# Performance work log

Hardware: AMD Instinct MI355X
Metric: run time of the kernel (lower is better)

## Reference

```python
import jax, jax.numpy as jnp
import numpy as np

N_NODES = 100000
D = 128
N_EDGES = 640000


def _spmm(edge_index, w, x, n):
    # out[i] = sum over edges (i<-j): w * x[j]
    src, dst = edge_index[0], edge_index[1]
    return jax.ops.segment_sum(w[:, None] * x[dst], src, num_segments=n)


def setup_inputs() -> dict:
    key = jax.random.key(0)
    ks = jax.random.split(key, 8)
    inp = {
        "index_vectors": jax.random.normal(ks[0], (N_NODES, D), dtype=jnp.float32),
        "edge_index1": jax.random.randint(ks[1], (2, N_EDGES), 0, N_NODES, dtype=jnp.int64),
        "w1": jnp.ones((N_EDGES,), dtype=jnp.float32),
        "edge_index2": jax.random.randint(ks[2], (2, N_EDGES), 0, N_NODES, dtype=jnp.int64),
        "w2": jnp.ones((N_EDGES,), dtype=jnp.float32),
        "edge_index3": jax.random.randint(ks[3], (2, N_EDGES), 0, N_NODES, dtype=jnp.int64),
        "w3": jnp.ones((N_EDGES,), dtype=jnp.float32),
        "zeroth": jax.random.uniform(ks[4], (1, 1), dtype=jnp.float32),
        "fst": jax.random.uniform(ks[5], (1, 1), dtype=jnp.float32),
        "snd": jax.random.uniform(ks[6], (1, 1), dtype=jnp.float32),
        "trd": jax.random.uniform(ks[7], (1, 1), dtype=jnp.float32),
    }
    return inp


def reference(index_vectors, edge_index1, w1, edge_index2, w2, edge_index3, w3,
              zeroth, fst, snd, trd):
    n = index_vectors.shape[0]
    # hop-1 context: A @ x
    fst_ctx = _spmm(edge_index1, w1, index_vectors, n)
    # hop-2 context: A^2 @ roll(x, 1, axis=1)   (permute_vecs=True)
    snd_ctx = _spmm(edge_index2, w2, jnp.roll(index_vectors, 1, axis=1), n)
    # hop-3 context: A^3 @ roll(x, 2, axis=1)
    trd_ctx = _spmm(edge_index3, w3, jnp.roll(index_vectors, 2, axis=1), n)

    # relu-normalized scalar order weights (get_orders)
    r0, r1, r2, r3 = (jax.nn.relu(zeroth), jax.nn.relu(fst),
                      jax.nn.relu(snd), jax.nn.relu(trd))
    tot = r0 + r1 + r2 + r3 + 1e-6
    r0, r1, r2, r3 = r0 / tot, r1 / tot, r2 / tot, r3 / tot

    # use_sign=False -> plain weighted combination
    return r0 * index_vectors + r1 * fst_ctx + r2 * snd_ctx + r3 * trd_ctx
```

## Files before the change

### kernel.cpp

```cpp
#include <hip/hip_runtime.h>

#define N_NODES 100000
#define D 128
#define N_EDGES 640000
#define TOT_EDGES (3 * N_EDGES)

#define NB   256
#define NPB  391
#define BCAP 9216
#define OVF_CAP 16384
#define EPB  3072
#define BINA_BLOCKS (TOT_EDGES / EPB)
#define EPT  (EPB / 256)
#define NKEY 2048

#define WS_OVFCNT 0
#define WS_BCUR   64
#define WS_BBASE  16448
#define WS_BNUM   17472
#define WS_OVF    18496
#define WS_TMP    280640
#define WS_FREC   19155008
#define WS_OFFS   34515008
#define WS_XB     34915016
#define WS_TOTAL_FAST 60515016

#ifndef __has_builtin
#define __has_builtin(x) 0
#endif
#if __has_builtin(__builtin_amdgcn_alignbit)
#define ALIGN16(hi, lo) __builtin_amdgcn_alignbit((hi), (lo), 16)
#else
#define ALIGN16(hi, lo) (((hi) << 16) | ((lo) >> 16))
#endif

__device__ __forceinline__ void load_r(const float* z0, const float* z1,
                                       const float* z2, const float* z3,
                                       float& r0, float& r1, float& r2, float& r3) {
    r0 = fmaxf(z0[0], 0.0f);
    r1 = fmaxf(z1[0], 0.0f);
    r2 = fmaxf(z2[0], 0.0f);
    r3 = fmaxf(z3[0], 0.0f);
    float inv = 1.0f / (r0 + r1 + r2 + r3 + 1e-6f);
    r0 *= inv; r1 *= inv; r2 *= inv; r3 *= inv;
}

__device__ __forceinline__ unsigned short bf16rn(float f) {
    unsigned int u = __float_as_uint(f);
    u += 0x7FFFu + ((u >> 16) & 1u);
    return (unsigned short)(u >> 16);
}

__global__ void cast_kernel(const float* __restrict__ x, ushort* __restrict__ xb) {
    int i = blockIdx.x * 256 + threadIdx.x;
    if (i >= N_NODES * D / 4) return;
    float4 v = ((const float4*)x)[i];
    ushort4 h;
    h.x = bf16rn(v.x); h.y = bf16rn(v.y); h.z = bf16rn(v.z); h.w = bf16rn(v.w);
    ((ushort4*)xb)[i] = h;
}

__global__ void binA_kernel(const int* __restrict__ ei1, const float* __restrict__ w1,
                            const int* __restrict__ ei2, const float* __restrict__ w2,
                            const int* __restrict__ ei3, const float* __restrict__ w3,
                            const float* __restrict__ z0, const float* __restrict__ z1,
                            const float* __restrict__ z2, const float* __restrict__ z3,
                            int* __restrict__ bcur, int* __restrict__ ovf_count,
                            int4* __restrict__ ovf, int2* __restrict__ tmp) {
    __shared__ int hist[NB];
    __shared__ int base[NB];
    int t = threadIdx.x;
    hist[t] = 0;
    __syncthreads();

    float r0, r1, r2, r3;
    load_r(z0, z1, z2, z3, r0, r1, r2, r3);

    int e0 = blockIdx.x * EPB;
    int rank[EPT];
    int bkt[EPT];
    int rxv[EPT];
    float scv[EPT];

#pragma unroll
    for (int k = 0; k < EPT; ++k) {
        int e = e0 + t + k * 256;
        int set = e / N_EDGES;
        int idx = e - set * N_EDGES;
        const int* ei;  const float* w;  float rk;
        if      (set == 0) { ei = ei1; w = w1; rk = r1; }
        else if (set == 1) { ei = ei2; w = w2; rk = r2; }
        else               { ei = ei3; w = w3; rk = r3; }
        int src = ei[idx];
        int dst = ei[N_EDGES + idx];
        int b = src / NPB;
        int local = src - b * NPB;
        bkt[k]  = b;
        rxv[k]  = dst | (set << 17) | (local << 19);
        scv[k]  = rk * w[idx];
        rank[k] = atomicAdd(&hist[b], 1);
    }
    __syncthreads();

    {
        int h = hist[t];
        base[t] = h ? atomicAdd(&bcur[t * 16], h) : 0;
    }
    __syncthreads();

#pragma unroll
    for (int k = 0; k < EPT; ++k) {
        int b = bkt[k];
        int pos = base[b] + rank[k];
        if (pos < BCAP) {
            tmp[(size_t)b * BCAP + pos] = make_int2(rxv[k], __float_as_int(scv[k]));
        } else {
            int o = atomicAdd(ovf_count, 1);
            int src = b * NPB + ((rxv[k] >> 19) & 0x1FF);
            if (o < OVF_CAP) ovf[o] = make_int4(src, rxv[k] & 0x7FFFF,
                                                __float_as_int(scv[k]), 0);
        }
    }
}

__global__ void scanB_kernel(const int* __restrict__ bcur,
                             int* __restrict__ bbase, int* __restrict__ bnum,
                             int* __restrict__ offsets) {
    __shared__ int s[NB];
    int t = threadIdx.x;
    int n = bcur[t * 16];
    if (n > BCAP) n = BCAP;
    bnum[t] = n;
    s[t] = n;
    __syncthreads();
    for (int off = 1; off < NB; off <<= 1) {
        int v = (t >= off) ? s[t - off] : 0;
        __syncthreads();
        s[t] += v;
        __syncthreads();
    }
    bbase[t] = s[t] - n;
    if (t == NB - 1) offsets[N_NODES] = s[t];
}

__global__ void binB_kernel(const int2* __restrict__ tmp,
                            const int* __restrict__ bbase, const int* __restrict__ bnum,
                            int2* __restrict__ frecs, int* __restrict__ offsets) {
    __shared__ int d[NKEY];
    __shared__ int ts[256];
    __shared__ int cur[NKEY];
    int b = blockIdx.x;
    int t = threadIdx.x;
    int n = bnum[b];
    int gbase = bbase[b];

    for (int i = t; i < NKEY; i += 256) d[i] = 0;
    __syncthreads();
    for (int i = t; i < n; i += 256) {
        int rx = tmp[(size_t)b * BCAP + i].x;
        int key = (((rx >> 19) & 0x1FF) << 2) | ((rx >> 17) & 3);
        atomicAdd(&d[key], 1);
    }
    __syncthreads();

    int loc[8];
    int tot = 0;
#pragma unroll
    for (int k = 0; k < 8; ++k) { loc[k] = tot; tot += d[8 * t + k]; }
    ts[t] = tot;
    __syncthreads();
    for (int off = 1; off < 256; off <<= 1) {
        int v = (t >= off) ? ts[t - off] : 0;
        __syncthreads();
        ts[t] += v;
        __syncthreads();
    }
    int tbase = ts[t] - tot;
#pragma unroll
    for (int k = 0; k < 8; ++k) cur[8 * t + k] = tbase + loc[k];
    __syncthreads();

    int node0 = b * NPB;
    for (int l = t; l < NPB; l += 256) {
        int node = node0 + l;
        if (node < N_NODES) offsets[node] = gbase + cur[l << 2];
    }
    __syncthreads();

    for (int i = t; i < n; i += 256) {
        int2 rec = tmp[(size_t)b * BCAP + i];
        int key = (((rec.x >> 19) & 0x1FF) << 2) | ((rec.x >> 17) & 3);
        int pos = atomicAdd(&cur[key], 1);
        frecs[gbase + pos] = make_int2(rec.x & 0x7FFFF, rec.y);
    }
}

#define GB_ACCUM(RX, RY)                                                       \
    {                                                                          \
        const uint4* rowp = (const uint4*)(xb + (size_t)((RX) & 0x1FFFF) * D); \
        uint4 v = rowp[l16];                                                   \
        int sh = ((RX) >> 17) & 3;                                             \
        float sc = __int_as_float(RY);                                         \
        unsigned int pw = (unsigned int)__shfl((int)v.w, prevq);               \
        unsigned int s1x = ALIGN16(v.x, pw);                                   \
        unsigned int s1y = ALIGN16(v.y, v.x);                                  \
        unsigned int s1z = ALIGN16(v.z, v.y);                                  \
        unsigned int s1w = ALIGN16(v.w, v.z);                                  \
        unsigned int u0 = (sh == 0) ? v.x : (sh == 1) ? s1x : pw;              \
        unsigned int u1 = (sh == 0) ? v.y : (sh == 1) ? s1y : v.x;             \
        unsigned int u2 = (sh == 0) ? v.z : (sh == 1) ? s1z : v.y;             \
        unsigned int u3 = (sh == 0) ? v.w : (sh == 1) ? s1w : v.z;             \
        acc0 += sc * __uint_as_float(u0 << 16);                                \
        acc1 += sc * __uint_as_float(u0 & 0xFFFF0000u);                        \
        acc2 += sc * __uint_as_float(u1 << 16);                                \
        acc3 += sc * __uint_as_float(u1 & 0xFFFF0000u);                        \
        acc4 += sc * __uint_as_float(u2 << 16);                                \
        acc5 += sc * __uint_as_float(u2 & 0xFFFF0000u);                        \
        acc6 += sc * __uint_as_float(u3 << 16);                                \
        acc7 += sc * __uint_as_float(u3 & 0xFFFF0000u);                        \
    }

__global__ void gatherb_kernel(const float* __restrict__ x,
                               const ushort* __restrict__ xb,
                               const int* __restrict__ offsets,
                               const int2* __restrict__ recs,
                               const float* __restrict__ z0, const float* __restrict__ z1,
                               const float* __restrict__ z2, const float* __restrict__ z3,
                               float* __restrict__ out) {
    int wid  = (blockIdx.x * blockDim.x + threadIdx.x) >> 6;
    int lane = threadIdx.x & 63;
    if (wid >= N_NODES) return;

    float r0, r1, r2, r3;
    load_r(z0, z1, z2, z3, r0, r1, r2, r3);

    int qt    = lane >> 4;
    int l16   = lane & 15;
    int prevq = (qt << 4) | ((l16 + 15) & 15);

    int beg = offsets[wid];
    int end = offsets[wid + 1];
    int count = end - beg;
    int cnt64 = (count < 64) ? count : 64;

    int mrx = 0, mry = 0;
    if (lane < cnt64) { int2 rec = recs[beg + lane]; mrx = rec.x; mry = rec.y; }

    float acc0 = 0.f, acc1 = 0.f, acc2 = 0.f, acc3 = 0.f;
    float acc4 = 0.f, acc5 = 0.f, acc6 = 0.f, acc7 = 0.f;

    for (int j = 0; j < cnt64; j += 4) {
        int srcl = j + qt;
        int rx = __shfl(mrx, srcl);
        int ry = __shfl(mry, srcl);
        GB_ACCUM(rx, ry)
    }
    for (int q = 64; q < count; q += 4) {
        int qq = q + qt;
        int rx = 0, ry = 0;
        if (qq < count) { int2 rec = recs[beg + qq]; rx = rec.x; ry = rec.y; }
        GB_ACCUM(rx, ry)
    }

    acc0 += __shfl_xor(acc0, 16); acc0 += __shfl_xor(acc0, 32);
    acc1 += __shfl_xor(acc1, 16); acc1 += __shfl_xor(acc1, 32);
    acc2 += __shfl_xor(acc2, 16); acc2 += __shfl_xor(acc2, 32);
    acc3 += __shfl_xor(acc3, 16); acc3 += __shfl_xor(acc3, 32);
    acc4 += __shfl_xor(acc4, 16); acc4 += __shfl_xor(acc4, 32);
    acc5 += __shfl_xor(acc5, 16); acc5 += __shfl_xor(acc5, 32);
    acc6 += __shfl_xor(acc6, 16); acc6 += __shfl_xor(acc6, 32);
    acc7 += __shfl_xor(acc7, 16); acc7 += __shfl_xor(acc7, 32);

    if (lane < 16) {
        const float4* xr = (const float4*)(x + (size_t)wid * D);
        float4 xlo = xr[2 * l16];
        float4 xhi = xr[2 * l16 + 1];
        float4 olo, ohi;
        olo.x = r0 * xlo.x + acc0;
        olo.y = r0 * xlo.y + acc1;
        olo.z = r0 * xlo.z + acc2;
        olo.w = r0 * xlo.w + acc3;
        ohi.x = r0 * xhi.x + acc4;
        ohi.y = r0 * xhi.y + acc5;
        ohi.z = r0 * xhi.z + acc6;
        ohi.w = r0 * xhi.w + acc7;
        float4* op = (float4*)(out + (size_t)wid * D);
        op[2 * l16]     = olo;
        op[2 * l16 + 1] = ohi;
    }
}

__global__ void ovf_kernel(const float* __restrict__ x,
                           const int* __restrict__ ovf_count,
                           const int4* __restrict__ ovf,
                           float* __restrict__ out) {
    int total_waves = (gridDim.x * blockDim.x) >> 6;
    int gw   = (blockIdx.x * blockDim.x + threadIdx.x) >> 6;
    int lane = threadIdx.x & 63;
    int n = *ovf_count;
    if (n > OVF_CAP) n = OVF_CAP;
    for (int r = gw; r < n; r += total_waves) {
        int4 rec = ovf[r];
        int src = rec.x;
        int dst = rec.y & 0x1FFFF;
        int sh  = (rec.y >> 17) & 3;
        float sc = __int_as_float(rec.z);
        const float* xr = x + (size_t)dst * D;
        float* orow = out + (size_t)src * D;
        int c0 = 2 * lane, c1 = 2 * lane + 1;
        atomicAdd(&orow[c0], sc * xr[(c0 - sh) & 127]);
        atomicAdd(&orow[c1], sc * xr[(c1 - sh) & 127]);
    }
}

#define SCAN_BLOCKS ((N_NODES + 255) / 256)
#define WS_COUNTS   0
#define WS_OFFSETS  400000
#define WS_CURSORS  800008
#define WS_BSUM     1200008
#define WS_BPRE     1201576
#define WS_RECS     1203144
#define WS_NEEDED_MID (WS_RECS + (size_t)TOT_EDGES * 8)

__global__ void hist_kernel(const int* __restrict__ ei1, const int* __restrict__ ei2,
                            const int* __restrict__ ei3, int* __restrict__ counts) {
    int e = blockIdx.x * blockDim.x + threadIdx.x;
    if (e >= TOT_EDGES) return;
    int set = e / N_EDGES;
    int idx = e - set * N_EDGES;
    const int* ei = (set == 0) ? ei1 : (set == 1) ? ei2 : ei3;
    atomicAdd(&counts[ei[idx]], 1);
}

__global__ void scan1_kernel(const int* __restrict__ counts,
                             int* __restrict__ offsets, int* __restrict__ bsum) {
    __shared__ int s[256];
    int t = threadIdx.x;
    int i = blockIdx.x * 256 + t;
    int v = (i < N_NODES) ? counts[i] : 0;
    s[t] = v;
    __syncthreads();
    for (int off = 1; off < 256; off <<= 1) {
        int u = (t >= off) ? s[t - off] : 0;
        __syncthreads();
        s[t] += u;
        __syncthreads();
    }
    if (i < N_NODES) offsets[i] = s[t] - v;
    if (t == 255) bsum[blockIdx.x] = s[255];
}

__global__ void scan2_kernel(const int* __restrict__ bsum, int* __restrict__ bpre) {
    __shared__ int s[512];
    int t = threadIdx.x;
    int v = (t < SCAN_BLOCKS) ? bsum[t] : 0;
    s[t] = v;
    __syncthreads();
    for (int off = 1; off < 512; off <<= 1) {
        int u = (t >= off) ? s[t - off] : 0;
        __syncthreads();
        s[t] += u;
        __syncthreads();
    }
    if (t < SCAN_BLOCKS) bpre[t] = s[t] - v;
}

__global__ void scan3_kernel(int* __restrict__ offsets, const int* __restrict__ bpre,
                             int* __restrict__ cursors) {
    int i = blockIdx.x * 256 + threadIdx.x;
    if (i < N_NODES) {
        int v = offsets[i] + bpre[blockIdx.x];
        offsets[i] = v;
        cursors[i] = v;
    }
    if (i == 0) offsets[N_NODES] = TOT_EDGES;
}

__global__ void fill_kernel(const int* __restrict__ ei1, const float* __restrict__ w1,
                            const int* __restrict__ ei2, const float* __restrict__ w2,
                            const int* __restrict__ ei3, const float* __restrict__ w3,
                            const float* __restrict__ z0, const float* __restrict__ z1,
                            const float* __restrict__ z2, const float* __restrict__ z3,
                            int* __restrict__ cursors, int2* __restrict__ recs) {
    int e = blockIdx.x * blockDim.x + threadIdx.x;
    if (e >= TOT_EDGES) return;
    int set = e / N_EDGES;
    int idx = e - set * N_EDGES;
    const int* ei;  const float* w;
    if      (set == 0) { ei = ei1; w = w1; }
    else if (set == 1) { ei = ei2; w = w2; }
    else               { ei = ei3; w = w3; }
    float r0, r1, r2, r3;
    load_r(z0, z1, z2, z3, r0, r1, r2, r3);
    float rk = (set == 0) ? r1 : (set == 1) ? r2 : r3;
    int src = ei[idx];
    int dst = ei[N_EDGES + idx];
    float scale = rk * w[idx];
    int pos = atomicAdd(&cursors[src], 1);
    recs[pos] = make_int2(dst | (set << 17), __float_as_int(scale));
}

__global__ void gatherd_kernel(const float* __restrict__ x,
                               const int* __restrict__ offsets,
                               const int2* __restrict__ recs,
                               const float* __restrict__ z0, const float* __restrict__ z1,
                               const float* __restrict__ z2, const float* __restrict__ z3,
                               float* __restrict__ out) {
    int wid  = (blockIdx.x * blockDim.x + threadIdx.x) >> 6;
    int lane = threadIdx.x & 63;
    if (wid >= N_NODES) return;
    float r0, r1, r2, r3;
    load_r(z0, z1, z2, z3, r0, r1, r2, r3);
    float2 xv = ((const float2*)(x + (size_t)wid * D))[lane];
    int beg = offsets[wid];
    int end = offsets[wid + 1];
    float2 a0 = {0.f, 0.f}, a1 = {0.f, 0.f}, a2 = {0.f, 0.f};
    for (int j = beg; j < end; ++j) {
        int2 rec = recs[j];
        float2 v = ((const float2*)(x + (size_t)(rec.x & 0x1FFFF) * D))[lane];
        int sh = (rec.x >> 17) & 3;
        float sc = __int_as_float(rec.y);
        if      (sh == 0) { a0.x += sc * v.x; a0.y += sc * v.y; }
        else if (sh == 1) { a1.x += sc * v.x; a1.y += sc * v.y; }
        else               { a2.x += sc * v.x; a2.y += sc * v.y; }
    }
    int prev = (lane + 63) & 63;
    float r1y = __shfl(a1.y, prev);
    float r2x = __shfl(a2.x, prev);
    float r2y = __shfl(a2.y, prev);
    float2 o;
    o.x = r0 * xv.x + a0.x + r1y  + r2x;
    o.y = r0 * xv.y + a0.y + a1.x + r2y;
    ((float2*)(out + (size_t)wid * D))[lane] = o;
}

extern "C" void kernel_launch(void* const* d_in, const int* in_sizes, int n_in,
                              void* d_out, int out_size, void* d_ws, size_t ws_size,
                              hipStream_t stream) {
    const float* x   = (const float*)d_in[0];
    const int*   ei1 = (const int*)  d_in[1];
    const float* w1  = (const float*)d_in[2];
    const int*   ei2 = (const int*)  d_in[3];
    const float* w2  = (const float*)d_in[4];
    const int*   ei3 = (const int*)  d_in[5];
    const float* w3  = (const float*)d_in[6];
    const float* z0  = (const float*)d_in[7];
    const float* z1  = (const float*)d_in[8];
    const float* z2  = (const float*)d_in[9];
    const float* z3  = (const float*)d_in[10];
    float* out = (float*)d_out;
    char* wsc = (char*)d_ws;

    if (ws_size >= WS_TOTAL_FAST) {
        int*    ovf_count = (int*)   (wsc + WS_OVFCNT);
        int*    bcur      = (int*)   (wsc + WS_BCUR);
        int*    bbase     = (int*)   (wsc + WS_BBASE);
        int*    bnum      = (int*)   (wsc + WS_BNUM);
        int4*   ovf       = (int4*)  (wsc + WS_OVF);
        int2*   tmp       = (int2*)  (wsc + WS_TMP);
        int2*   frecs     = (int2*)  (wsc + WS_FREC);
        int*    offsets   = (int*)   (wsc + WS_OFFS);
        ushort* xb        = (ushort*)(wsc + WS_XB);

        hipMemsetAsync(wsc, 0, WS_BBASE, stream);
        cast_kernel<<<(N_NODES * D / 4 + 255) / 256, 256, 0, stream>>>(x, xb);
        binA_kernel<<<BINA_BLOCKS, 256, 0, stream>>>(ei1, w1, ei2, w2, ei3, w3,
                                                     z0, z1, z2, z3,
                                                     bcur, ovf_count, ovf, tmp);
        scanB_kernel<<<1, NB, 0, stream>>>(bcur, bbase, bnum, offsets);
        binB_kernel<<<NB, 256, 0, stream>>>(tmp, bbase, bnum, frecs, offsets);
        gatherb_kernel<<<(N_NODES * 64 + 255) / 256, 256, 0, stream>>>(x, xb, offsets,
                                                                       frecs, z0, z1, z2, z3,
                                                                       out);
        ovf_kernel<<<128, 256, 0, stream>>>(x, ovf_count, ovf, out);
    } else {
        int*  counts  = (int*) (wsc + WS_COUNTS);
        int*  offsets = (int*) (wsc + WS_OFFSETS);
        int*  cursors = (int*) (wsc + WS_CURSORS);
        int*  bsum    = (int*) (wsc + WS_BSUM);
        int*  bpre    = (int*) (wsc + WS_BPRE);
        int2* recs    = (int2*)(wsc + WS_RECS);

        hipMemsetAsync(counts, 0, N_NODES * sizeof(int), stream);
        hist_kernel<<<TOT_EDGES / 256, 256, 0, stream>>>(ei1, ei2, ei3, counts);
        scan1_kernel<<<SCAN_BLOCKS, 256, 0, stream>>>(counts, offsets, bsum);
        scan2_kernel<<<1, 512, 0, stream>>>(bsum, bpre);
        scan3_kernel<<<SCAN_BLOCKS, 256, 0, stream>>>(offsets, bpre, cursors);
        fill_kernel<<<TOT_EDGES / 256, 256, 0, stream>>>(ei1, w1, ei2, w2, ei3, w3,
                                                         z0, z1, z2, z3, cursors, recs);
        gatherd_kernel<<<(N_NODES * 64 + 255) / 256, 256, 0, stream>>>(x, offsets, recs,
                                                                       z0, z1, z2, z3, out);
    }
}
```

Before: 280.3 us.

## Fuse cast into binning, fold scan into binB, use finer buckets, unroll gather

The bf16 cast and the first binning pass now run as one launch. The single-block bucket scan is removed and each binB block recomputes the prefix over bucket counts itself. Buckets grow from 256 to 1024, each holding fewer nodes, which spreads the sort across more, smaller blocks. The gather loop now issues two row loads per iteration to raise memory-level parallelism. Together these cut two launches and serial passes, at the cost of redundant scans in every binB block and more global atomics during binning.

```diff
diff --git a/kernel.cpp b/kernel.cpp
--- a/kernel.cpp
+++ b/kernel.cpp
@@ -5,25 +5,24 @@
 #define N_EDGES 640000
 #define TOT_EDGES (3 * N_EDGES)
 
-#define NB   256
-#define NPB  391
-#define BCAP 9216
+#define NB   1024
+#define NPB  98
+#define BCAP 2304
 #define OVF_CAP 16384
 #define EPB  3072
 #define BINA_BLOCKS (TOT_EDGES / EPB)
 #define EPT  (EPB / 256)
-#define NKEY 2048
+#define NKEY 512
+#define CAST_BLOCKS ((N_NODES * D / 4 + 255) / 256)
 
 #define WS_OVFCNT 0
 #define WS_BCUR   64
-#define WS_BBASE  16448
-#define WS_BNUM   17472
-#define WS_OVF    18496
-#define WS_TMP    280640
-#define WS_FREC   19155008
-#define WS_OFFS   34515008
-#define WS_XB     34915016
-#define WS_TOTAL_FAST 60515016
+#define WS_OVF    65600
+#define WS_TMP    327744
+#define WS_FREC   19202112
+#define WS_OFFS   34562112
+#define WS_XB     34962120
+#define WS_TOTAL_FAST 60562120
 
 #ifndef __has_builtin
 #define __has_builtin(x) 0
@@ -51,26 +50,29 @@
     return (unsigned short)(u >> 16);
 }
 
-__global__ void cast_kernel(const float* __restrict__ x, ushort* __restrict__ xb) {
-    int i = blockIdx.x * 256 + threadIdx.x;
-    if (i >= N_NODES * D / 4) return;
-    float4 v = ((const float4*)x)[i];
-    ushort4 h;
-    h.x = bf16rn(v.x); h.y = bf16rn(v.y); h.z = bf16rn(v.z); h.w = bf16rn(v.w);
-    ((ushort4*)xb)[i] = h;
-}
-
-__global__ void binA_kernel(const int* __restrict__ ei1, const float* __restrict__ w1,
-                            const int* __restrict__ ei2, const float* __restrict__ w2,
-                            const int* __restrict__ ei3, const float* __restrict__ w3,
-                            const float* __restrict__ z0, const float* __restrict__ z1,
-                            const float* __restrict__ z2, const float* __restrict__ z3,
-                            int* __restrict__ bcur, int* __restrict__ ovf_count,
-                            int4* __restrict__ ovf, int2* __restrict__ tmp) {
+__global__ __launch_bounds__(256) void prep_kernel(
+        const float* __restrict__ x, ushort* __restrict__ xb,
+        const int* __restrict__ ei1, const float* __restrict__ w1,
+        const int* __restrict__ ei2, const float* __restrict__ w2,
+        const int* __restrict__ ei3, const float* __restrict__ w3,
+        const float* __restrict__ z0, const float* __restrict__ z1,
+        const float* __restrict__ z2, const float* __restrict__ z3,
+        int* __restrict__ bcur, int* __restrict__ ovf_count,
+        int4* __restrict__ ovf, int2* __restrict__ tmp) {
+    if (blockIdx.x >= BINA_BLOCKS) {
+        int i = (blockIdx.x - BINA_BLOCKS) * 256 + threadIdx.x;
+        if (i < N_NODES * D / 4) {
+            float4 v = ((const float4*)x)[i];
+            ushort4 h;
+            h.x = bf16rn(v.x); h.y = bf16rn(v.y); h.z = bf16rn(v.z); h.w = bf16rn(v.w);
+            ((ushort4*)xb)[i] = h;
+        }
+        return;
+    }
     __shared__ int hist[NB];
     __shared__ int base[NB];
     int t = threadIdx.x;
-    hist[t] = 0;
+    for (int i = t; i < NB; i += 256) hist[i] = 0;
     __syncthreads();
 
     float r0, r1, r2, r3;
@@ -102,9 +104,9 @@
     }
     __syncthreads();
 
-    {
-        int h = hist[t];
-        base[t] = h ? atomicAdd(&bcur[t * 16], h) : 0;
+    for (int i = t; i < NB; i += 256) {
+        int h = hist[i];
+        base[i] = h ? atomicAdd(&bcur[i * 16], h) : 0;
     }
     __syncthreads();
 
@@ -116,57 +118,64 @@
             tmp[(size_t)b * BCAP + pos] = make_int2(rxv[k], __float_as_int(scv[k]));
         } else {
             int o = atomicAdd(ovf_count, 1);
-            int src = b * NPB + ((rxv[k] >> 19) & 0x1FF);
+            int src = b * NPB + ((rxv[k] >> 19) & 0x7F);
             if (o < OVF_CAP) ovf[o] = make_int4(src, rxv[k] & 0x7FFFF,
                                                 __float_as_int(scv[k]), 0);
         }
     }
 }
 
-__global__ void scanB_kernel(const int* __restrict__ bcur,
-                             int* __restrict__ bbase, int* __restrict__ bnum,
-                             int* __restrict__ offsets) {
-    __shared__ int s[NB];
-    int t = threadIdx.x;
-    int n = bcur[t * 16];
-    if (n > BCAP) n = BCAP;
-    bnum[t] = n;
-    s[t] = n;
-    __syncthreads();
-    for (int off = 1; off < NB; off <<= 1) {
-        int v = (t >= off) ? s[t - off] : 0;
-        __syncthreads();
-        s[t] += v;
-        __syncthreads();
-    }
-    bbase[t] = s[t] - n;
-    if (t == NB - 1) offsets[N_NODES] = s[t];
-}
-
-__global__ void binB_kernel(const int2* __restrict__ tmp,
-                            const int* __restrict__ bbase, const int* __restrict__ bnum,
-                            int2* __restrict__ frecs, int* __restrict__ offsets) {
+__global__ __launch_bounds__(256) void binB_kernel(
+        const int* __restrict__ bcur, const int2* __restrict__ tmp,
+        int2* __restrict__ frecs, int* __restrict__ offsets) {
+    __shared__ int sc4[256];
     __shared__ int d[NKEY];
     __shared__ int ts[256];
     __shared__ int cur[NKEY];
+    __shared__ int sh_gbase, sh_n;
     int b = blockIdx.x;
     int t = threadIdx.x;
-    int n = bnum[b];
-    int gbase = bbase[b];
-
-    for (int i = t; i < NKEY; i += 256) d[i] = 0;
-    __syncthreads();
+
+    d[t] = 0; d[t + 256] = 0;
+
+    int v4[4];
+    int cex[4];
+    int tsum = 0;
+#pragma unroll
+    for (int k = 0; k < 4; ++k) {
+        int g = 4 * t + k;
+        int v = bcur[g * 16];
+        if (v > BCAP) v = BCAP;
+        cex[k] = tsum;
+        tsum += v;
+        v4[k] = v;
+    }
+    sc4[t] = tsum;
+    __syncthreads();
+    for (int off = 1; off < 256; off <<= 1) {
+        int v = (t >= off) ? sc4[t - off] : 0;
+        __syncthreads();
+        sc4[t] += v;
+        __syncthreads();
+    }
+    if (t == (b >> 2)) {
+        sh_gbase = sc4[t] - tsum + cex[b & 3];
+        sh_n     = v4[b & 3];
+    }
+    if (b == NB - 1 && t == 255) offsets[N_NODES] = sc4[255];
+    __syncthreads();
+    int gbase = sh_gbase;
+    int n     = sh_n;
+
     for (int i = t; i < n; i += 256) {
         int rx = tmp[(size_t)b * BCAP + i].x;
-        int key = (((rx >> 19) & 0x1FF) << 2) | ((rx >> 17) & 3);
+        int key = (((rx >> 19) & 0x7F) << 2) | ((rx >> 17) & 3);
         atomicAdd(&d[key], 1);
     }
     __syncthreads();
 
-    int loc[8];
-    int tot = 0;
-#pragma unroll
-    for (int k = 0; k < 8; ++k) { loc[k] = tot; tot += d[8 * t + k]; }
+    int k0 = d[2 * t], k1 = d[2 * t + 1];
+    int tot = k0 + k1;
     ts[t] = tot;
     __syncthreads();
     for (int off = 1; off < 256; off <<= 1) {
@@ -176,40 +185,37 @@
         __syncthreads();
     }
     int tbase = ts[t] - tot;
-#pragma unroll
-    for (int k = 0; k < 8; ++k) cur[8 * t + k] = tbase + loc[k];
-    __syncthreads();
-
-    int node0 = b * NPB;
-    for (int l = t; l < NPB; l += 256) {
-        int node = node0 + l;
-        if (node < N_NODES) offsets[node] = gbase + cur[l << 2];
+    cur[2 * t]     = tbase;
+    cur[2 * t + 1] = tbase + k0;
+    __syncthreads();
+
+    if (t < NPB) {
+        int node = b * NPB + t;
+        if (node < N_NODES) offsets[node] = gbase + cur[t << 2];
     }
     __syncthreads();
 
     for (int i = t; i < n; i += 256) {
         int2 rec = tmp[(size_t)b * BCAP + i];
-        int key = (((rec.x >> 19) & 0x1FF) << 2) | ((rec.x >> 17) & 3);
+        int key = (((rec.x >> 19) & 0x7F) << 2) | ((rec.x >> 17) & 3);
         int pos = atomicAdd(&cur[key], 1);
         frecs[gbase + pos] = make_int2(rec.x & 0x7FFFF, rec.y);
     }
 }
 
-#define GB_ACCUM(RX, RY)                                                       \
+#define GB_ACC(V, RX, RY)                                                      \
     {                                                                          \
-        const uint4* rowp = (const uint4*)(xb + (size_t)((RX) & 0x1FFFF) * D); \
-        uint4 v = rowp[l16];                                                   \
         int sh = ((RX) >> 17) & 3;                                             \
         float sc = __int_as_float(RY);                                         \
-        unsigned int pw = (unsigned int)__shfl((int)v.w, prevq);               \
-        unsigned int s1x = ALIGN16(v.x, pw);                                   \
-        unsigned int s1y = ALIGN16(v.y, v.x);                                  \
-        unsigned int s1z = ALIGN16(v.z, v.y);                                  \
-        unsigned int s1w = ALIGN16(v.w, v.z);                                  \
-        unsigned int u0 = (sh == 0) ? v.x : (sh == 1) ? s1x : pw;              \
-        unsigned int u1 = (sh == 0) ? v.y : (sh == 1) ? s1y : v.x;             \
-        unsigned int u2 = (sh == 0) ? v.z : (sh == 1) ? s1z : v.y;             \
-        unsigned int u3 = (sh == 0) ? v.w : (sh == 1) ? s1w : v.z;             \
+        unsigned int pw = (unsigned int)__shfl((int)(V).w, prevq);             \
+        unsigned int s1x = ALIGN16((V).x, pw);                                 \
+        unsigned int s1y = ALIGN16((V).y, (V).x);                              \
+        unsigned int s1z = ALIGN16((V).z, (V).y);                              \
+        unsigned int s1w = ALIGN16((V).w, (V).z);                              \
+        unsigned int u0 = (sh == 0) ? (V).x : (sh == 1) ? s1x : pw;            \
+        unsigned int u1 = (sh == 0) ? (V).y : (sh == 1) ? s1y : (V).x;         \
+        unsigned int u2 = (sh == 0) ? (V).z : (sh == 1) ? s1z : (V).y;         \
+        unsigned int u3 = (sh == 0) ? (V).w : (sh == 1) ? s1w : (V).z;         \
         acc0 += sc * __uint_as_float(u0 << 16);                                \
         acc1 += sc * __uint_as_float(u0 & 0xFFFF0000u);                        \
         acc2 += sc * __uint_as_float(u1 << 16);                                \
@@ -220,13 +226,12 @@
         acc7 += sc * __uint_as_float(u3 & 0xFFFF0000u);                        \
     }
 
-__global__ void gatherb_kernel(const float* __restrict__ x,
-                               const ushort* __restrict__ xb,
-                               const int* __restrict__ offsets,
-                               const int2* __restrict__ recs,
-                               const float* __restrict__ z0, const float* __restrict__ z1,
-                               const float* __restrict__ z2, const float* __restrict__ z3,
-                               float* __restrict__ out) {
+__global__ __launch_bounds__(256) void gatherb_kernel(
+        const float* __restrict__ x, const ushort* __restrict__ xb,
+        const int* __restrict__ offsets, const int2* __restrict__ recs,
+        const float* __restrict__ z0, const float* __restrict__ z1,
+        const float* __restrict__ z2, const float* __restrict__ z3,
+        float* __restrict__ out) {
     int wid  = (blockIdx.x * blockDim.x + threadIdx.x) >> 6;
     int lane = threadIdx.x & 63;
     if (wid >= N_NODES) return;
@@ -249,17 +254,25 @@
     float acc0 = 0.f, acc1 = 0.f, acc2 = 0.f, acc3 = 0.f;
     float acc4 = 0.f, acc5 = 0.f, acc6 = 0.f, acc7 = 0.f;
 
-    for (int j = 0; j < cnt64; j += 4) {
-        int srcl = j + qt;
-        int rx = __shfl(mrx, srcl);
-        int ry = __shfl(mry, srcl);
-        GB_ACCUM(rx, ry)
+    for (int j = 0; j < cnt64; j += 8) {
+        int sa = j + qt;
+        int sb = j + 4 + qt;
+        int rxa = __shfl(mrx, sa), rya = __shfl(mry, sa);
+        int rxb = __shfl(mrx, sb), ryb = __shfl(mry, sb);
+        const uint4* pa = (const uint4*)(xb + (size_t)(rxa & 0x1FFFF) * D);
+        const uint4* pb = (const uint4*)(xb + (size_t)(rxb & 0x1FFFF) * D);
+        uint4 va = pa[l16];
+        uint4 vb = pb[l16];
+        GB_ACC(va, rxa, rya)
+        GB_ACC(vb, rxb, ryb)
     }
     for (int q = 64; q < count; q += 4) {
         int qq = q + qt;
         int rx = 0, ry = 0;
         if (qq < count) { int2 rec = recs[beg + qq]; rx = rec.x; ry = rec.y; }
-        GB_ACCUM(rx, ry)
+        const uint4* pp = (const uint4*)(xb + (size_t)(rx & 0x1FFFF) * D);
+        uint4 vv = pp[l16];
+        GB_ACC(vv, rx, ry)
     }
 
     acc0 += __shfl_xor(acc0, 16); acc0 += __shfl_xor(acc0, 32);
@@ -454,21 +467,17 @@
     if (ws_size >= WS_TOTAL_FAST) {
         int*    ovf_count = (int*)   (wsc + WS_OVFCNT);
         int*    bcur      = (int*)   (wsc + WS_BCUR);
-        int*    bbase     = (int*)   (wsc + WS_BBASE);
-        int*    bnum      = (int*)   (wsc + WS_BNUM);
         int4*   ovf       = (int4*)  (wsc + WS_OVF);
         int2*   tmp       = (int2*)  (wsc + WS_TMP);
         int2*   frecs     = (int2*)  (wsc + WS_FREC);
         int*    offsets   = (int*)   (wsc + WS_OFFS);
         ushort* xb        = (ushort*)(wsc + WS_XB);
 
-        hipMemsetAsync(wsc, 0, WS_BBASE, stream);
-        cast_kernel<<<(N_NODES * D / 4 + 255) / 256, 256, 0, stream>>>(x, xb);
-        binA_kernel<<<BINA_BLOCKS, 256, 0, stream>>>(ei1, w1, ei2, w2, ei3, w3,
-                                                     z0, z1, z2, z3,
-                                                     bcur, ovf_count, ovf, tmp);
-        scanB_kernel<<<1, NB, 0, stream>>>(bcur, bbase, bnum, offsets);
-        binB_kernel<<<NB, 256, 0, stream>>>(tmp, bbase, bnum, frecs, offsets);
+        hipMemsetAsync(wsc, 0, WS_OVF, stream);
+        prep_kernel<<<BINA_BLOCKS + CAST_BLOCKS, 256, 0, stream>>>(
+            x, xb, ei1, w1, ei2, w2, ei3, w3, z0, z1, z2, z3,
+            bcur, ovf_count, ovf, tmp);
+        binB_kernel<<<NB, 256, 0, stream>>>(bcur, tmp, frecs, offsets);
         gatherb_kernel<<<(N_NODES * 64 + 255) / 256, 256, 0, stream>>>(x, xb, offsets,
                                                                        frecs, z0, z1, z2, z3,
                                                                        out);
```

New measurement: 282.1 us. About the same (+0.7%).
